# Performance work log

Hardware: AMD Instinct MI355X
Metric: run time of the kernel (lower is better)

Reference implementation:

```python
import jax, jax.numpy as jnp
import numpy as np

B, N, E, H, D, F = 2, 4096, 128, 8, 16, 512
EPS = 1e-6


def _rms_norm(x, w):
    xf = x.astype(jnp.float32)
    n = xf * jax.lax.rsqrt(jnp.mean(xf * xf, axis=-1, keepdims=True) + EPS)
    return n.astype(x.dtype) * w


def setup_inputs() -> dict:
    key = jax.random.key(0)
    ks = jax.random.split(key, 12)
    s = 1.0 / np.sqrt(E)
    sf = 1.0 / np.sqrt(F)
    coords = jax.random.uniform(ks[10], (B, N, 2))
    dis = jnp.sqrt(jnp.sum((coords[:, :, None, :] - coords[:, None, :, :]) ** 2, -1))
    dis = dis * (1.0 - jnp.eye(N))  # zero diagonal
    return {
        "input1": jax.random.normal(ks[0], (B, N, E), jnp.float32),
        "dis_matrix": dis.astype(jnp.float32),
        "Wq": jax.random.uniform(ks[1], (E, E), jnp.float32, -s, s),
        "Wk": jax.random.uniform(ks[2], (E, E), jnp.float32, -s, s),
        "Wv": jax.random.uniform(ks[3], (E, E), jnp.float32, -s, s),
        "alpha": jnp.float32(1.0),
        "ln1_w": jnp.ones((E,), jnp.float32),
        "ln2_w": jnp.ones((E,), jnp.float32),
        "Wcomb": jax.random.uniform(ks[4], (E, E), jnp.float32, -s, s),
        "W1": jax.random.uniform(ks[5], (F, E), jnp.float32, -s, s),
        "b1": jax.random.uniform(ks[6], (F,), jnp.float32, -s, s),
        "W2": jax.random.uniform(ks[7], (E, F), jnp.float32, -sf, sf),
        "b2": jax.random.uniform(ks[8], (E,), jnp.float32, -sf, sf),
    }


def _sparse_attention_afm(x, dis_matrix, Wq, Wk, Wv, alpha):
    # project and split heads: [B,N,E] -> [B,H,N,D]
    def heads(w):
        return (x @ w.T).reshape(B, N, H, D).transpose(0, 2, 1, 3)
    q, k, v = heads(Wq), heads(Wk), heads(Wv)
    log2n = jnp.float32(np.log2(N))
    dis_weight = jnp.exp(-alpha * log2n * dis_matrix)  # [B,N,N] (i,j)
    k_weight = jnp.exp(k)  # [B,H,N,D]
    w1 = jnp.einsum('bij,bhik->bhjk', dis_weight, k_weight * v)
    w2 = jnp.einsum('bij,bhik->bhjk', dis_weight, k_weight)
    out = jax.nn.sigmoid(q) * (w1 / w2)  # [B,H,N,D]
    return out.transpose(0, 2, 1, 3).reshape(B, N, E)


def reference(input1, dis_matrix, Wq, Wk, Wv, alpha, ln1_w, ln2_w, Wcomb, W1, b1, W2, b2):
    h = _rms_norm(input1, ln1_w)
    attn = _sparse_attention_afm(h, dis_matrix, Wq, Wk, Wv, alpha)
    out1 = input1 + attn @ Wcomb.T
    h2 = _rms_norm(out1, ln2_w)
    ffn = jax.nn.relu(h2 @ W1.T + b1) @ W2.T + b2
    return out1 + ffn
```

## Files before the change

### kernel.cpp

```cpp
#include <hip/hip_runtime.h>

#define NTOK 4096
#define BNROWS 8192
#define EDIM 128
#define FDIM 512

typedef __attribute__((ext_vector_type(8))) short bf16x8;
typedef __attribute__((ext_vector_type(4))) float f32x4;

__device__ __forceinline__ ushort f2bf(float x) {
    union { float f; unsigned u; } c; c.f = x;
    unsigned r = c.u + 0x7FFF + ((c.u >> 16) & 1);
    return (ushort)(r >> 16);
}

__global__ void prep_k(const float* __restrict__ Wq, const float* __restrict__ Wk,
                       const float* __restrict__ Wv, const float* __restrict__ Wc,
                       const float* __restrict__ W1, const float* __restrict__ W2,
                       ushort* __restrict__ Wbf,
                       const float* __restrict__ input1, const float* __restrict__ ln1w,
                       ushort* __restrict__ h_bf) {
    const int bx = blockIdx.x, t = threadIdx.x;
    if (bx < 768) {
        int i = bx * 256 + t;
        const float* src; int off;
        if (i < 16384)       { src = Wq; off = i; }
        else if (i < 32768)  { src = Wk; off = i - 16384; }
        else if (i < 49152)  { src = Wv; off = i - 32768; }
        else if (i < 65536)  { src = Wc; off = i - 49152; }
        else if (i < 131072) { src = W1; off = i - 65536; }
        else                 { src = W2; off = i - 131072; }
        Wbf[i] = f2bf(src[off]);
    } else {
        int row  = (bx - 768) * 4 + (t >> 6);
        int lane = t & 63;
        float2 v = ((const float2*)(input1 + (size_t)row * EDIM))[lane];
        float ss = v.x * v.x + v.y * v.y;
#pragma unroll
        for (int off = 32; off > 0; off >>= 1) ss += __shfl_down(ss, off, 64);
        ss = __shfl(ss, 0, 64);
        float r = rsqrtf(ss * (1.0f / 128.0f) + 1e-6f);
        float2 wv = ((const float2*)ln1w)[lane];
        ushort2 o; o.x = f2bf(v.x * r * wv.x); o.y = f2bf(v.y * r * wv.y);
        ((ushort2*)(h_bf + (size_t)row * EDIM))[lane] = o;
    }
}

#define EB_SIGQ  0
#define EB_RELUB 1
#define EB_ACC   2

template<int EPIL>
__device__ __forceinline__ void mgemm_body(
    const ushort* __restrict__ A, int lda,
    const ushort* __restrict__ B, int ldb,
    float* __restrict__ outF, ushort* __restrict__ outB, int Nout, int colbase,
    const float* __restrict__ bias, int M0, int nchunks)
{
    __shared__ ushort As[32 * 136];
    __shared__ ushort Bs[128 * 136];
    const int t = threadIdx.x, lane = t & 63, wv = t >> 6;
    const int m15 = lane & 15, kq = (lane >> 4) * 8;
    const int c0w = wv * 32;
    f32x4 acc[2][2] = {};

    const int ar = t >> 3, as0 = (t & 7) * 2;
    const int br = t >> 1, bs0 = (t & 1) * 8;

    for (int c = 0; c < nchunks; ++c) {
        if (c) __syncthreads();
        int kb = c * 128;
#pragma unroll
        for (int j = 0; j < 2; ++j) {
            int seg = as0 + j;
            *(bf16x8*)&As[ar * 136 + seg * 8] =
                *(const bf16x8*)&A[(size_t)(M0 + ar) * lda + kb + seg * 8];
        }
#pragma unroll
        for (int j = 0; j < 8; ++j) {
            int seg = bs0 + j;
            *(bf16x8*)&Bs[br * 136 + seg * 8] =
                *(const bf16x8*)&B[(size_t)br * ldb + kb + seg * 8];
        }
        __syncthreads();
#pragma unroll
        for (int kc = 0; kc < 4; ++kc) {
            int ko = kc * 32 + kq;
            bf16x8 a0 = *(const bf16x8*)&As[m15 * 136 + ko];
            bf16x8 a1 = *(const bf16x8*)&As[(16 + m15) * 136 + ko];
            bf16x8 b0 = *(const bf16x8*)&Bs[(c0w + m15) * 136 + ko];
            bf16x8 b1 = *(const bf16x8*)&Bs[(c0w + 16 + m15) * 136 + ko];
            acc[0][0] = __builtin_amdgcn_mfma_f32_16x16x32_bf16(a0, b0, acc[0][0], 0, 0, 0);
            acc[0][1] = __builtin_amdgcn_mfma_f32_16x16x32_bf16(a0, b1, acc[0][1], 0, 0, 0);
            acc[1][0] = __builtin_amdgcn_mfma_f32_16x16x32_bf16(a1, b0, acc[1][0], 0, 0, 0);
            acc[1][1] = __builtin_amdgcn_mfma_f32_16x16x32_bf16(a1, b1, acc[1][1], 0, 0, 0);
        }
    }
#pragma unroll
    for (int mi = 0; mi < 2; ++mi)
#pragma unroll
        for (int ni = 0; ni < 2; ++ni)
#pragma unroll
            for (int r = 0; r < 4; ++r) {
                int row = M0 + mi * 16 + (lane >> 4) * 4 + r;
                int lc  = c0w + ni * 16 + m15;
                size_t off = (size_t)row * Nout + colbase + lc;
                float vv = acc[mi][ni][r];
                if (EPIL == EB_SIGQ)  outF[off] = 1.0f / (1.0f + __expf(-vv));
                if (EPIL == EB_RELUB) outB[off] = f2bf(fmaxf(vv + bias[lc], 0.0f));
                if (EPIL == EB_ACC)   outF[off] += vv;
            }
}

__launch_bounds__(256, 3)
__global__ void q_sig_k(const ushort* __restrict__ h, const ushort* __restrict__ Wbf,
                        float* __restrict__ sigq) {
    mgemm_body<EB_SIGQ>(h, 128, Wbf, 128, sigq, nullptr, 128, 0, nullptr,
                        blockIdx.x * 32, 1);
}

__launch_bounds__(256, 3)
__global__ void ffn1_k(const ushort* __restrict__ h2, const ushort* __restrict__ Wbf,
                       const float* __restrict__ b1, ushort* __restrict__ mid) {
    int N0 = blockIdx.y * 128;
    mgemm_body<EB_RELUB>(h2, 128, Wbf + 65536 + N0 * 128, 128, nullptr, mid, 512, N0,
                         b1 + N0, blockIdx.x * 32, 1);
}

__launch_bounds__(256, 3)
__global__ void ffn2_k(const ushort* __restrict__ mid, const ushort* __restrict__ Wbf,
                       float* __restrict__ outp) {
    mgemm_body<EB_ACC>(mid, 512, Wbf + 131072, 512, outp, nullptr, 128, 0, nullptr,
                       blockIdx.x * 32, 4);
}

__launch_bounds__(256, 3)
__global__ void kv_mt_k(const ushort* __restrict__ h, const ushort* __restrict__ Wbf,
                        ushort* __restrict__ Mt) {
    __shared__ ushort As[32 * 136];
    __shared__ ushort Bs[2][64 * 136];
    const int t = threadIdx.x, lane = t & 63, wv = t >> 6;
    const int m15 = lane & 15, quad = lane >> 4, kq = quad * 8;
    const int M0 = blockIdx.x * 32;
    const int e0 = blockIdx.y * 64;

    const int ar = t >> 3, as0 = (t & 7) * 2;
#pragma unroll
    for (int j = 0; j < 2; ++j) {
        int seg = as0 + j;
        *(bf16x8*)&As[ar * 136 + seg * 8] =
            *(const bf16x8*)&h[(size_t)(M0 + ar) * 128 + seg * 8];
    }
    const int bm = t >> 7;
    const int br = (t & 127) >> 1, bs0 = (t & 1) * 8;
    const ushort* W = Wbf + 16384 + bm * 16384;
#pragma unroll
    for (int j = 0; j < 8; ++j) {
        int seg = bs0 + j;
        *(bf16x8*)&Bs[bm][br * 136 + seg * 8] =
            *(const bf16x8*)&W[(size_t)(e0 + br) * 128 + seg * 8];
    }
    __syncthreads();

    f32x4 acck[2] = {}, accv[2] = {};
    const int cw = wv * 16;
#pragma unroll
    for (int kc = 0; kc < 4; ++kc) {
        int ko = kc * 32 + kq;
        bf16x8 a0 = *(const bf16x8*)&As[m15 * 136 + ko];
        bf16x8 a1 = *(const bf16x8*)&As[(16 + m15) * 136 + ko];
        bf16x8 bk = *(const bf16x8*)&Bs[0][(cw + m15) * 136 + ko];
        bf16x8 bv = *(const bf16x8*)&Bs[1][(cw + m15) * 136 + ko];
        acck[0] = __builtin_amdgcn_mfma_f32_16x16x32_bf16(a0, bk, acck[0], 0, 0, 0);
        acck[1] = __builtin_amdgcn_mfma_f32_16x16x32_bf16(a1, bk, acck[1], 0, 0, 0);
        accv[0] = __builtin_amdgcn_mfma_f32_16x16x32_bf16(a0, bv, accv[0], 0, 0, 0);
        accv[1] = __builtin_amdgcn_mfma_f32_16x16x32_bf16(a1, bv, accv[1], 0, 0, 0);
    }
    const int b  = M0 >> 12;
    const int i0 = M0 & (NTOK - 1);
    const int e  = e0 + cw + m15;
    ushort* mt0 = Mt + ((size_t)b * 256 + e) * NTOK;
    ushort* mt1 = Mt + ((size_t)b * 256 + 128 + e) * NTOK;
#pragma unroll
    for (int mi = 0; mi < 2; ++mi) {
        int ib = i0 + mi * 16 + quad * 4;
        ushort4 pv, pk;
        float kw0 = __expf(acck[mi][0]); pv.x = f2bf(kw0 * accv[mi][0]); pk.x = f2bf(kw0);
        float kw1 = __expf(acck[mi][1]); pv.y = f2bf(kw1 * accv[mi][1]); pk.y = f2bf(kw1);
        float kw2 = __expf(acck[mi][2]); pv.z = f2bf(kw2 * accv[mi][2]); pk.z = f2bf(kw2);
        float kw3 = __expf(acck[mi][3]); pv.w = f2bf(kw3 * accv[mi][3]); pk.w = f2bf(kw3);
        *(ushort4*)&mt0[ib] = pv;
        *(ushort4*)&mt1[ib] = pk;
    }
}

__launch_bounds__(256, 2)
__global__ void big_gemm_k(const float* __restrict__ dis, const float* __restrict__ alphap,
                           const ushort* __restrict__ Mt,
                           float* __restrict__ P0, float* __restrict__ P1) {
    __shared__ ushort As[32 * 72];
    __shared__ ushort Bs[256 * 72];
    const int t = threadIdx.x, lane = t & 63, wv = t >> 6;
    const int m15 = lane & 15, quad = lane >> 4, kq = quad * 8;
    const int j0 = blockIdx.x * 32;
    const int b  = blockIdx.y;
    const int s  = blockIdx.z;
    const float coef = -alphap[0] * 12.0f;
    const float* disb = dis + (size_t)b * NTOK * NTOK;
    const ushort* Mtb = Mt + (size_t)b * 256 * NTOK;
    float* outp = ((s == 0) ? P0 : P1) + (size_t)b * NTOK * 256;

    f32x4 acc[2][4] = {};
    const int aj = t >> 3, ak = (t & 7) * 8;
    const int brow = t >> 3, bseg = (t & 7) * 8;
    const int k0 = s * (NTOK / 2);

    float4 fa0, fa1;
    bf16x8 pb[8];
    {
        const float* ap = disb + (size_t)(j0 + aj) * NTOK + k0 + ak;
        fa0 = *(const float4*)ap; fa1 = *(const float4*)(ap + 4);
#pragma unroll
        for (int p = 0; p < 8; ++p)
            pb[p] = *(const bf16x8*)&Mtb[(size_t)(p * 32 + brow) * NTOK + k0 + bseg];
    }

    for (int it = 0; it < 32; ++it) {
        bf16x8 a8;
        a8[0] = (short)f2bf(__expf(coef * fa0.x));
        a8[1] = (short)f2bf(__expf(coef * fa0.y));
        a8[2] = (short)f2bf(__expf(coef * fa0.z));
        a8[3] = (short)f2bf(__expf(coef * fa0.w));
        a8[4] = (short)f2bf(__expf(coef * fa1.x));
        a8[5] = (short)f2bf(__expf(coef * fa1.y));
        a8[6] = (short)f2bf(__expf(coef * fa1.z));
        a8[7] = (short)f2bf(__expf(coef * fa1.w));
        *(bf16x8*)&As[aj * 72 + ak] = a8;
#pragma unroll
        for (int p = 0; p < 8; ++p)
            *(bf16x8*)&Bs[(p * 32 + brow) * 72 + bseg] = pb[p];
        __syncthreads();
        if (it < 31) {
            int kn = k0 + (it + 1) * 64;
            const float* ap = disb + (size_t)(j0 + aj) * NTOK + kn + ak;
            fa0 = *(const float4*)ap; fa1 = *(const float4*)(ap + 4);
#pragma unroll
            for (int p = 0; p < 8; ++p)
                pb[p] = *(const bf16x8*)&Mtb[(size_t)(p * 32 + brow) * NTOK + kn + bseg];
        }
#pragma unroll
        for (int kh = 0; kh < 2; ++kh) {
            int ko = kh * 32 + kq;
            bf16x8 a0 = *(const bf16x8*)&As[m15 * 72 + ko];
            bf16x8 a1 = *(const bf16x8*)&As[(16 + m15) * 72 + ko];
#pragma unroll
            for (int ni = 0; ni < 4; ++ni) {
                bf16x8 bv = *(const bf16x8*)&Bs[(wv * 64 + ni * 16 + m15) * 72 + ko];
                acc[0][ni] = __builtin_amdgcn_mfma_f32_16x16x32_bf16(a0, bv, acc[0][ni], 0, 0, 0);
                acc[1][ni] = __builtin_amdgcn_mfma_f32_16x16x32_bf16(a1, bv, acc[1][ni], 0, 0, 0);
            }
        }
        __syncthreads();
    }
#pragma unroll
    for (int mi = 0; mi < 2; ++mi)
#pragma unroll
        for (int ni = 0; ni < 4; ++ni)
#pragma unroll
            for (int r = 0; r < 4; ++r) {
                int j = j0 + mi * 16 + quad * 4 + r;
                int c = wv * 64 + ni * 16 + m15;
                outp[(size_t)j * 256 + c] = acc[mi][ni][r];
            }
}

__launch_bounds__(256, 2)
__global__ void wcomb_rms2_k(const float* __restrict__ sigq,
                             const float* __restrict__ P0, const float* __restrict__ P1,
                             const ushort* __restrict__ Wbf,
                             const float* __restrict__ input1, const float* __restrict__ b2,
                             const float* __restrict__ ln2w,
                             float* __restrict__ outD, ushort* __restrict__ h2) {
    __shared__ ushort As[32 * 136];
    __shared__ ushort Bs[128 * 136];
    __shared__ float  O[32][132];
    const int t = threadIdx.x, lane = t & 63, wv = t >> 6;
    const int m15 = lane & 15, quad = lane >> 4, kq = quad * 8;
    const int M0 = blockIdx.x * 32;

    {
        const int ar = t >> 3, e0 = (t & 7) * 16;
        const int g = M0 + ar;
        const float4* sg = (const float4*)(sigq + (size_t)g * 128 + e0);
        const float4* p0a = (const float4*)(P0 + (size_t)g * 256 + e0);
        const float4* p1a = (const float4*)(P1 + (size_t)g * 256 + e0);
        const float4* p0b = (const float4*)(P0 + (size_t)g * 256 + 128 + e0);
        const float4* p1b = (const float4*)(P1 + (size_t)g * 256 + 128 + e0);
#pragma unroll
        for (int i = 0; i < 4; ++i) {
            float4 s = sg[i];
            float4 u0 = p0a[i], u1 = p1a[i], d0 = p0b[i], d1 = p1b[i];
            ushort4 a;
            a.x = f2bf(s.x * (u0.x + u1.x) / (d0.x + d1.x));
            a.y = f2bf(s.y * (u0.y + u1.y) / (d0.y + d1.y));
            a.z = f2bf(s.z * (u0.z + u1.z) / (d0.z + d1.z));
            a.w = f2bf(s.w * (u0.w + u1.w) / (d0.w + d1.w));
            *(ushort4*)&As[ar * 136 + e0 + i * 4] = a;
        }
    }
    {
        const int br = t >> 1, bs0 = (t & 1) * 8;
        const ushort* W = Wbf + 49152;
#pragma unroll
        for (int j = 0; j < 8; ++j) {
            int seg = bs0 + j;
            *(bf16x8*)&Bs[br * 136 + seg * 8] =
                *(const bf16x8*)&W[(size_t)br * 128 + seg * 8];
        }
    }
    __syncthreads();

    f32x4 acc[2][2] = {};
    const int c0w = wv * 32;
#pragma unroll
    for (int kc = 0; kc < 4; ++kc) {
        int ko = kc * 32 + kq;
        bf16x8 a0 = *(const bf16x8*)&As[m15 * 136 + ko];
        bf16x8 a1 = *(const bf16x8*)&As[(16 + m15) * 136 + ko];
        bf16x8 b0 = *(const bf16x8*)&Bs[(c0w + m15) * 136 + ko];
        bf16x8 b1 = *(const bf16x8*)&Bs[(c0w + 16 + m15) * 136 + ko];
        acc[0][0] = __builtin_amdgcn_mfma_f32_16x16x32_bf16(a0, b0, acc[0][0], 0, 0, 0);
        acc[0][1] = __builtin_amdgcn_mfma_f32_16x16x32_bf16(a0, b1, acc[0][1], 0, 0, 0);
        acc[1][0] = __builtin_amdgcn_mfma_f32_16x16x32_bf16(a1, b0, acc[1][0], 0, 0, 0);
        acc[1][1] = __builtin_amdgcn_mfma_f32_16x16x32_bf16(a1, b1, acc[1][1], 0, 0, 0);
    }
#pragma unroll
    for (int mi = 0; mi < 2; ++mi)
#pragma unroll
        for (int ni = 0; ni < 2; ++ni)
#pragma unroll
            for (int r = 0; r < 4; ++r) {
                int rl = mi * 16 + quad * 4 + r;
                int col = c0w + ni * 16 + m15;
                size_t off = (size_t)(M0 + rl) * 128 + col;
                float v = acc[mi][ni][r] + input1[off];
                O[rl][col] = v;
                outD[off] = v + b2[col];
            }
    __syncthreads();
    {
        const int row = t >> 3, seg = t & 7;
        float4 x[4];
        float ss = 0.f;
#pragma unroll
        for (int i = 0; i < 4; ++i) {
            x[i] = *(const float4*)&O[row][seg * 16 + i * 4];
            ss += x[i].x * x[i].x + x[i].y * x[i].y + x[i].z * x[i].z + x[i].w * x[i].w;
        }
        ss += __shfl_down(ss, 4, 8);
        ss += __shfl_down(ss, 2, 8);
        ss += __shfl_down(ss, 1, 8);
        ss = __shfl(ss, 0, 8);
        float rr = rsqrtf(ss * (1.0f / 128.0f) + 1e-6f);
        ushort* hp = h2 + (size_t)(M0 + row) * 128 + seg * 16;
#pragma unroll
        for (int i = 0; i < 4; ++i) {
            float4 wv4 = *(const float4*)&ln2w[seg * 16 + i * 4];
            ushort4 o;
            o.x = f2bf(x[i].x * rr * wv4.x);
            o.y = f2bf(x[i].y * rr * wv4.y);
            o.z = f2bf(x[i].z * rr * wv4.z);
            o.w = f2bf(x[i].w * rr * wv4.w);
            *(ushort4*)&hp[i * 4] = o;
        }
    }
}

extern "C" void kernel_launch(void* const* d_in, const int* in_sizes, int n_in,
                              void* d_out, int out_size, void* d_ws, size_t ws_size,
                              hipStream_t stream) {
    const float* input1 = (const float*)d_in[0];
    const float* dis    = (const float*)d_in[1];
    const float* Wq     = (const float*)d_in[2];
    const float* Wk     = (const float*)d_in[3];
    const float* Wv     = (const float*)d_in[4];
    const float* alpha  = (const float*)d_in[5];
    const float* ln1    = (const float*)d_in[6];
    const float* ln2    = (const float*)d_in[7];
    const float* Wcomb  = (const float*)d_in[8];
    const float* W1     = (const float*)d_in[9];
    const float* b1     = (const float*)d_in[10];
    const float* W2     = (const float*)d_in[11];
    const float* b2     = (const float*)d_in[12];
    float* out = (float*)d_out;

    char* w8 = (char*)d_ws;
    ushort* Wbf  = (ushort*)(w8);
    ushort* h_bf = (ushort*)(w8 + (1u << 20));
    float*  sigq = (float*)(w8 + (4u << 20));
    ushort* Mt   = (ushort*)(w8 + (8u << 20));
    float*  P0   = (float*)(w8 + (12u << 20));
    float*  P1   = (float*)(w8 + (20u << 20));
    ushort* h2   = (ushort*)(w8 + (1u << 20));
    ushort* mid  = (ushort*)(w8 + (12u << 20));

    prep_k<<<dim3(2816), 256, 0, stream>>>(Wq, Wk, Wv, Wcomb, W1, W2, Wbf,
                                           input1, ln1, h_bf);
    q_sig_k<<<dim3(256), 256, 0, stream>>>(h_bf, Wbf, sigq);
    kv_mt_k<<<dim3(256, 2), 256, 0, stream>>>(h_bf, Wbf, Mt);
    big_gemm_k<<<dim3(128, 2, 2), 256, 0, stream>>>(dis, alpha, Mt, P0, P1);
    wcomb_rms2_k<<<dim3(256), 256, 0, stream>>>(sigq, P0, P1, Wbf, input1, b2,
                                                ln2, out, h2);
    ffn1_k<<<dim3(256, 4), 256, 0, stream>>>(h2, Wbf, b1, mid);
    ffn2_k<<<dim3(256), 256, 0, stream>>>(mid, Wbf, out);
}
```

Measured before the change: 268.1 us.

## Fuse RMSNorm+QKV projection, fuse FFN, split big GEMM K four ways

Combines the weight conversion, RMSNorm1, Q/K/V projections and sigmoid/exp epilogues into one kernel that converts Wq/Wk/Wv to bf16 on the fly in shared memory. FFN1 and FFN2 are merged into one kernel that keeps the ReLU intermediate in LDS. The distance GEMM splits its reduction into four parts instead of two to double the block count and raise occupancy. The combine kernel now sums four partials. Together this cuts launches and global round trips, at the cost of more partial-sum traffic and redundant per-block weight conversion.

```diff
diff --git a/kernel.cpp b/kernel.cpp
--- a/kernel.cpp
+++ b/kernel.cpp
@@ -14,190 +14,124 @@
     return (ushort)(r >> 16);
 }
 
-__global__ void prep_k(const float* __restrict__ Wq, const float* __restrict__ Wk,
-                       const float* __restrict__ Wv, const float* __restrict__ Wc,
-                       const float* __restrict__ W1, const float* __restrict__ W2,
-                       ushort* __restrict__ Wbf,
-                       const float* __restrict__ input1, const float* __restrict__ ln1w,
-                       ushort* __restrict__ h_bf) {
+__launch_bounds__(256, 1)
+__global__ void qkv_k(const float* __restrict__ input1, const float* __restrict__ ln1w,
+                      const float* __restrict__ Wq, const float* __restrict__ Wk,
+                      const float* __restrict__ Wv, const float* __restrict__ Wc,
+                      const float* __restrict__ W1, const float* __restrict__ W2,
+                      ushort* __restrict__ Wbf, float* __restrict__ sigq,
+                      ushort* __restrict__ Mt) {
     const int bx = blockIdx.x, t = threadIdx.x;
-    if (bx < 768) {
-        int i = bx * 256 + t;
-        const float* src; int off;
-        if (i < 16384)       { src = Wq; off = i; }
-        else if (i < 32768)  { src = Wk; off = i - 16384; }
-        else if (i < 49152)  { src = Wv; off = i - 32768; }
-        else if (i < 65536)  { src = Wc; off = i - 49152; }
-        else if (i < 131072) { src = W1; off = i - 65536; }
-        else                 { src = W2; off = i - 131072; }
-        Wbf[i] = f2bf(src[off]);
-    } else {
-        int row  = (bx - 768) * 4 + (t >> 6);
-        int lane = t & 63;
-        float2 v = ((const float2*)(input1 + (size_t)row * EDIM))[lane];
-        float ss = v.x * v.x + v.y * v.y;
-#pragma unroll
-        for (int off = 32; off > 0; off >>= 1) ss += __shfl_down(ss, off, 64);
-        ss = __shfl(ss, 0, 64);
-        float r = rsqrtf(ss * (1.0f / 128.0f) + 1e-6f);
-        float2 wv = ((const float2*)ln1w)[lane];
-        ushort2 o; o.x = f2bf(v.x * r * wv.x); o.y = f2bf(v.y * r * wv.y);
-        ((ushort2*)(h_bf + (size_t)row * EDIM))[lane] = o;
-    }
-}
-
-#define EB_SIGQ  0
-#define EB_RELUB 1
-#define EB_ACC   2
-
-template<int EPIL>
-__device__ __forceinline__ void mgemm_body(
-    const ushort* __restrict__ A, int lda,
-    const ushort* __restrict__ B, int ldb,
-    float* __restrict__ outF, ushort* __restrict__ outB, int Nout, int colbase,
-    const float* __restrict__ bias, int M0, int nchunks)
-{
+    if (bx >= 256) {
+        int off = (bx - 256) * 1024 + t * 4;
+        const float* src; int o2;
+        if (off < 16384)      { src = Wc; o2 = off; }
+        else if (off < 81920) { src = W1; o2 = off - 16384; }
+        else                  { src = W2; o2 = off - 81920; }
+        float4 f = *(const float4*)(src + o2);
+        ushort4 u; u.x = f2bf(f.x); u.y = f2bf(f.y); u.z = f2bf(f.z); u.w = f2bf(f.w);
+        *(ushort4*)(Wbf + off) = u;
+        return;
+    }
     __shared__ ushort As[32 * 136];
-    __shared__ ushort Bs[128 * 136];
-    const int t = threadIdx.x, lane = t & 63, wv = t >> 6;
-    const int m15 = lane & 15, kq = (lane >> 4) * 8;
+    __shared__ ushort Bs[3][128 * 136];
+    const int lane = t & 63, wv = t >> 6;
+    const int m15 = lane & 15, quad = lane >> 4, kq = quad * 8;
+    const int M0 = bx * 32;
+
+    {
+        const int ar = t >> 3, c0 = (t & 7) * 16;
+        const float* xr = input1 + (size_t)(M0 + ar) * EDIM + c0;
+        float4 x[4];
+        float ss = 0.f;
+#pragma unroll
+        for (int i = 0; i < 4; ++i) {
+            x[i] = ((const float4*)xr)[i];
+            ss += x[i].x * x[i].x + x[i].y * x[i].y + x[i].z * x[i].z + x[i].w * x[i].w;
+        }
+        ss += __shfl_down(ss, 4, 8);
+        ss += __shfl_down(ss, 2, 8);
+        ss += __shfl_down(ss, 1, 8);
+        ss = __shfl(ss, 0, 8);
+        float rr = rsqrtf(ss * (1.0f / 128.0f) + 1e-6f);
+#pragma unroll
+        for (int i = 0; i < 4; ++i) {
+            float4 wv4 = *(const float4*)&ln1w[c0 + i * 4];
+            ushort4 o;
+            o.x = f2bf(x[i].x * rr * wv4.x);
+            o.y = f2bf(x[i].y * rr * wv4.y);
+            o.z = f2bf(x[i].z * rr * wv4.z);
+            o.w = f2bf(x[i].w * rr * wv4.w);
+            *(ushort4*)&As[ar * 136 + c0 + i * 4] = o;
+        }
+    }
+    {
+        const int br = t >> 1, half = (t & 1) * 64;
+        const float* srcs[3] = {Wq, Wk, Wv};
+#pragma unroll
+        for (int m = 0; m < 3; ++m) {
+            const float* wsrc = srcs[m] + (size_t)br * 128 + half;
+#pragma unroll
+            for (int j = 0; j < 8; ++j) {
+                float4 f0 = *(const float4*)(wsrc + j * 8);
+                float4 f1 = *(const float4*)(wsrc + j * 8 + 4);
+                bf16x8 u;
+                u[0] = (short)f2bf(f0.x); u[1] = (short)f2bf(f0.y);
+                u[2] = (short)f2bf(f0.z); u[3] = (short)f2bf(f0.w);
+                u[4] = (short)f2bf(f1.x); u[5] = (short)f2bf(f1.y);
+                u[6] = (short)f2bf(f1.z); u[7] = (short)f2bf(f1.w);
+                *(bf16x8*)&Bs[m][br * 136 + half + j * 8] = u;
+            }
+        }
+    }
+    __syncthreads();
+
+    f32x4 aq[2][2] = {}, ak[2][2] = {}, av[2][2] = {};
     const int c0w = wv * 32;
-    f32x4 acc[2][2] = {};
-
-    const int ar = t >> 3, as0 = (t & 7) * 2;
-    const int br = t >> 1, bs0 = (t & 1) * 8;
-
-    for (int c = 0; c < nchunks; ++c) {
-        if (c) __syncthreads();
-        int kb = c * 128;
-#pragma unroll
-        for (int j = 0; j < 2; ++j) {
-            int seg = as0 + j;
-            *(bf16x8*)&As[ar * 136 + seg * 8] =
-                *(const bf16x8*)&A[(size_t)(M0 + ar) * lda + kb + seg * 8];
-        }
-#pragma unroll
-        for (int j = 0; j < 8; ++j) {
-            int seg = bs0 + j;
-            *(bf16x8*)&Bs[br * 136 + seg * 8] =
-                *(const bf16x8*)&B[(size_t)br * ldb + kb + seg * 8];
-        }
-        __syncthreads();
-#pragma unroll
-        for (int kc = 0; kc < 4; ++kc) {
-            int ko = kc * 32 + kq;
-            bf16x8 a0 = *(const bf16x8*)&As[m15 * 136 + ko];
-            bf16x8 a1 = *(const bf16x8*)&As[(16 + m15) * 136 + ko];
-            bf16x8 b0 = *(const bf16x8*)&Bs[(c0w + m15) * 136 + ko];
-            bf16x8 b1 = *(const bf16x8*)&Bs[(c0w + 16 + m15) * 136 + ko];
-            acc[0][0] = __builtin_amdgcn_mfma_f32_16x16x32_bf16(a0, b0, acc[0][0], 0, 0, 0);
-            acc[0][1] = __builtin_amdgcn_mfma_f32_16x16x32_bf16(a0, b1, acc[0][1], 0, 0, 0);
-            acc[1][0] = __builtin_amdgcn_mfma_f32_16x16x32_bf16(a1, b0, acc[1][0], 0, 0, 0);
-            acc[1][1] = __builtin_amdgcn_mfma_f32_16x16x32_bf16(a1, b1, acc[1][1], 0, 0, 0);
-        }
-    }
-#pragma unroll
-    for (int mi = 0; mi < 2; ++mi)
-#pragma unroll
-        for (int ni = 0; ni < 2; ++ni)
-#pragma unroll
-            for (int r = 0; r < 4; ++r) {
-                int row = M0 + mi * 16 + (lane >> 4) * 4 + r;
-                int lc  = c0w + ni * 16 + m15;
-                size_t off = (size_t)row * Nout + colbase + lc;
-                float vv = acc[mi][ni][r];
-                if (EPIL == EB_SIGQ)  outF[off] = 1.0f / (1.0f + __expf(-vv));
-                if (EPIL == EB_RELUB) outB[off] = f2bf(fmaxf(vv + bias[lc], 0.0f));
-                if (EPIL == EB_ACC)   outF[off] += vv;
-            }
-}
-
-__launch_bounds__(256, 3)
-__global__ void q_sig_k(const ushort* __restrict__ h, const ushort* __restrict__ Wbf,
-                        float* __restrict__ sigq) {
-    mgemm_body<EB_SIGQ>(h, 128, Wbf, 128, sigq, nullptr, 128, 0, nullptr,
-                        blockIdx.x * 32, 1);
-}
-
-__launch_bounds__(256, 3)
-__global__ void ffn1_k(const ushort* __restrict__ h2, const ushort* __restrict__ Wbf,
-                       const float* __restrict__ b1, ushort* __restrict__ mid) {
-    int N0 = blockIdx.y * 128;
-    mgemm_body<EB_RELUB>(h2, 128, Wbf + 65536 + N0 * 128, 128, nullptr, mid, 512, N0,
-                         b1 + N0, blockIdx.x * 32, 1);
-}
-
-__launch_bounds__(256, 3)
-__global__ void ffn2_k(const ushort* __restrict__ mid, const ushort* __restrict__ Wbf,
-                       float* __restrict__ outp) {
-    mgemm_body<EB_ACC>(mid, 512, Wbf + 131072, 512, outp, nullptr, 128, 0, nullptr,
-                       blockIdx.x * 32, 4);
-}
-
-__launch_bounds__(256, 3)
-__global__ void kv_mt_k(const ushort* __restrict__ h, const ushort* __restrict__ Wbf,
-                        ushort* __restrict__ Mt) {
-    __shared__ ushort As[32 * 136];
-    __shared__ ushort Bs[2][64 * 136];
-    const int t = threadIdx.x, lane = t & 63, wv = t >> 6;
-    const int m15 = lane & 15, quad = lane >> 4, kq = quad * 8;
-    const int M0 = blockIdx.x * 32;
-    const int e0 = blockIdx.y * 64;
-
-    const int ar = t >> 3, as0 = (t & 7) * 2;
-#pragma unroll
-    for (int j = 0; j < 2; ++j) {
-        int seg = as0 + j;
-        *(bf16x8*)&As[ar * 136 + seg * 8] =
-            *(const bf16x8*)&h[(size_t)(M0 + ar) * 128 + seg * 8];
-    }
-    const int bm = t >> 7;
-    const int br = (t & 127) >> 1, bs0 = (t & 1) * 8;
-    const ushort* W = Wbf + 16384 + bm * 16384;
-#pragma unroll
-    for (int j = 0; j < 8; ++j) {
-        int seg = bs0 + j;
-        *(bf16x8*)&Bs[bm][br * 136 + seg * 8] =
-            *(const bf16x8*)&W[(size_t)(e0 + br) * 128 + seg * 8];
-    }
-    __syncthreads();
-
-    f32x4 acck[2] = {}, accv[2] = {};
-    const int cw = wv * 16;
 #pragma unroll
     for (int kc = 0; kc < 4; ++kc) {
         int ko = kc * 32 + kq;
         bf16x8 a0 = *(const bf16x8*)&As[m15 * 136 + ko];
         bf16x8 a1 = *(const bf16x8*)&As[(16 + m15) * 136 + ko];
-        bf16x8 bk = *(const bf16x8*)&Bs[0][(cw + m15) * 136 + ko];
-        bf16x8 bv = *(const bf16x8*)&Bs[1][(cw + m15) * 136 + ko];
-        acck[0] = __builtin_amdgcn_mfma_f32_16x16x32_bf16(a0, bk, acck[0], 0, 0, 0);
-        acck[1] = __builtin_amdgcn_mfma_f32_16x16x32_bf16(a1, bk, acck[1], 0, 0, 0);
-        accv[0] = __builtin_amdgcn_mfma_f32_16x16x32_bf16(a0, bv, accv[0], 0, 0, 0);
-        accv[1] = __builtin_amdgcn_mfma_f32_16x16x32_bf16(a1, bv, accv[1], 0, 0, 0);
+#pragma unroll
+        for (int ni = 0; ni < 2; ++ni) {
+            int brow = (c0w + ni * 16 + m15) * 136 + ko;
+            bf16x8 bq = *(const bf16x8*)&Bs[0][brow];
+            bf16x8 bk = *(const bf16x8*)&Bs[1][brow];
+            bf16x8 bv = *(const bf16x8*)&Bs[2][brow];
+            aq[0][ni] = __builtin_amdgcn_mfma_f32_16x16x32_bf16(a0, bq, aq[0][ni], 0, 0, 0);
+            aq[1][ni] = __builtin_amdgcn_mfma_f32_16x16x32_bf16(a1, bq, aq[1][ni], 0, 0, 0);
+            ak[0][ni] = __builtin_amdgcn_mfma_f32_16x16x32_bf16(a0, bk, ak[0][ni], 0, 0, 0);
+            ak[1][ni] = __builtin_amdgcn_mfma_f32_16x16x32_bf16(a1, bk, ak[1][ni], 0, 0, 0);
+            av[0][ni] = __builtin_amdgcn_mfma_f32_16x16x32_bf16(a0, bv, av[0][ni], 0, 0, 0);
+            av[1][ni] = __builtin_amdgcn_mfma_f32_16x16x32_bf16(a1, bv, av[1][ni], 0, 0, 0);
+        }
     }
     const int b  = M0 >> 12;
     const int i0 = M0 & (NTOK - 1);
-    const int e  = e0 + cw + m15;
-    ushort* mt0 = Mt + ((size_t)b * 256 + e) * NTOK;
-    ushort* mt1 = Mt + ((size_t)b * 256 + 128 + e) * NTOK;
-#pragma unroll
-    for (int mi = 0; mi < 2; ++mi) {
-        int ib = i0 + mi * 16 + quad * 4;
-        ushort4 pv, pk;
-        float kw0 = __expf(acck[mi][0]); pv.x = f2bf(kw0 * accv[mi][0]); pk.x = f2bf(kw0);
-        float kw1 = __expf(acck[mi][1]); pv.y = f2bf(kw1 * accv[mi][1]); pk.y = f2bf(kw1);
-        float kw2 = __expf(acck[mi][2]); pv.z = f2bf(kw2 * accv[mi][2]); pk.z = f2bf(kw2);
-        float kw3 = __expf(acck[mi][3]); pv.w = f2bf(kw3 * accv[mi][3]); pk.w = f2bf(kw3);
-        *(ushort4*)&mt0[ib] = pv;
-        *(ushort4*)&mt1[ib] = pk;
-    }
-}
-
-__launch_bounds__(256, 2)
+#pragma unroll
+    for (int mi = 0; mi < 2; ++mi)
+#pragma unroll
+        for (int ni = 0; ni < 2; ++ni) {
+            int e  = c0w + ni * 16 + m15;
+            int ib = i0 + mi * 16 + quad * 4;
+#pragma unroll
+            for (int r = 0; r < 4; ++r)
+                sigq[(size_t)(M0 + mi * 16 + quad * 4 + r) * EDIM + e] =
+                    1.0f / (1.0f + __expf(-aq[mi][ni][r]));
+            ushort4 pv, pk;
+            float k0 = __expf(ak[mi][ni][0]); pv.x = f2bf(k0 * av[mi][ni][0]); pk.x = f2bf(k0);
+            float k1 = __expf(ak[mi][ni][1]); pv.y = f2bf(k1 * av[mi][ni][1]); pk.y = f2bf(k1);
+            float k2 = __expf(ak[mi][ni][2]); pv.z = f2bf(k2 * av[mi][ni][2]); pk.z = f2bf(k2);
+            float k3 = __expf(ak[mi][ni][3]); pv.w = f2bf(k3 * av[mi][ni][3]); pk.w = f2bf(k3);
+            *(ushort4*)&Mt[((size_t)b * 256 + e) * NTOK + ib]       = pv;
+            *(ushort4*)&Mt[((size_t)b * 256 + 128 + e) * NTOK + ib] = pk;
+        }
+}
+
+__launch_bounds__(256, 3)
 __global__ void big_gemm_k(const float* __restrict__ dis, const float* __restrict__ alphap,
-                           const ushort* __restrict__ Mt,
-                           float* __restrict__ P0, float* __restrict__ P1) {
+                           const ushort* __restrict__ Mt, float* __restrict__ P) {
     __shared__ ushort As[32 * 72];
     __shared__ ushort Bs[256 * 72];
     const int t = threadIdx.x, lane = t & 63, wv = t >> 6;
@@ -208,12 +142,13 @@
     const float coef = -alphap[0] * 12.0f;
     const float* disb = dis + (size_t)b * NTOK * NTOK;
     const ushort* Mtb = Mt + (size_t)b * 256 * NTOK;
-    float* outp = ((s == 0) ? P0 : P1) + (size_t)b * NTOK * 256;
+    float* outp = P + ((size_t)(s * 2 + b) * NTOK + j0) * 256;
 
     f32x4 acc[2][4] = {};
     const int aj = t >> 3, ak = (t & 7) * 8;
     const int brow = t >> 3, bseg = (t & 7) * 8;
-    const int k0 = s * (NTOK / 2);
+    const int k0 = s * (NTOK / 4);
+    const int nIter = (NTOK / 4) / 64;
 
     float4 fa0, fa1;
     bf16x8 pb[8];
@@ -225,7 +160,7 @@
             pb[p] = *(const bf16x8*)&Mtb[(size_t)(p * 32 + brow) * NTOK + k0 + bseg];
     }
 
-    for (int it = 0; it < 32; ++it) {
+    for (int it = 0; it < nIter; ++it) {
         bf16x8 a8;
         a8[0] = (short)f2bf(__expf(coef * fa0.x));
         a8[1] = (short)f2bf(__expf(coef * fa0.y));
@@ -240,7 +175,7 @@
         for (int p = 0; p < 8; ++p)
             *(bf16x8*)&Bs[(p * 32 + brow) * 72 + bseg] = pb[p];
         __syncthreads();
-        if (it < 31) {
+        if (it < nIter - 1) {
             int kn = k0 + (it + 1) * 64;
             const float* ap = disb + (size_t)(j0 + aj) * NTOK + kn + ak;
             fa0 = *(const float4*)ap; fa1 = *(const float4*)(ap + 4);
@@ -268,15 +203,14 @@
         for (int ni = 0; ni < 4; ++ni)
 #pragma unroll
             for (int r = 0; r < 4; ++r) {
-                int j = j0 + mi * 16 + quad * 4 + r;
+                int j = mi * 16 + quad * 4 + r;
                 int c = wv * 64 + ni * 16 + m15;
                 outp[(size_t)j * 256 + c] = acc[mi][ni][r];
             }
 }
 
 __launch_bounds__(256, 2)
-__global__ void wcomb_rms2_k(const float* __restrict__ sigq,
-                             const float* __restrict__ P0, const float* __restrict__ P1,
+__global__ void wcomb_rms2_k(const float* __restrict__ sigq, const float* __restrict__ P,
                              const ushort* __restrict__ Wbf,
                              const float* __restrict__ input1, const float* __restrict__ b2,
                              const float* __restrict__ ln2w,
@@ -291,32 +225,37 @@
     {
         const int ar = t >> 3, e0 = (t & 7) * 16;
         const int g = M0 + ar;
-        const float4* sg = (const float4*)(sigq + (size_t)g * 128 + e0);
-        const float4* p0a = (const float4*)(P0 + (size_t)g * 256 + e0);
-        const float4* p1a = (const float4*)(P1 + (size_t)g * 256 + e0);
-        const float4* p0b = (const float4*)(P0 + (size_t)g * 256 + 128 + e0);
-        const float4* p1b = (const float4*)(P1 + (size_t)g * 256 + 128 + e0);
+        const int b = g >> 12, j = g & (NTOK - 1);
+        const float* sg = sigq + (size_t)g * 128 + e0;
+        const float* Pg0 = P + ((size_t)(0 + b) * NTOK + j) * 256 + e0;
+        const float* Pg1 = P + ((size_t)(2 + b) * NTOK + j) * 256 + e0;
+        const float* Pg2 = P + ((size_t)(4 + b) * NTOK + j) * 256 + e0;
+        const float* Pg3 = P + ((size_t)(6 + b) * NTOK + j) * 256 + e0;
 #pragma unroll
         for (int i = 0; i < 4; ++i) {
-            float4 s = sg[i];
-            float4 u0 = p0a[i], u1 = p1a[i], d0 = p0b[i], d1 = p1b[i];
+            float4 s = *(const float4*)(sg + i * 4);
+            float4 n0 = *(const float4*)(Pg0 + i * 4);
+            float4 n1 = *(const float4*)(Pg1 + i * 4);
+            float4 n2 = *(const float4*)(Pg2 + i * 4);
+            float4 n3 = *(const float4*)(Pg3 + i * 4);
+            float4 d0 = *(const float4*)(Pg0 + 128 + i * 4);
+            float4 d1 = *(const float4*)(Pg1 + 128 + i * 4);
+            float4 d2 = *(const float4*)(Pg2 + 128 + i * 4);
+            float4 d3 = *(const float4*)(Pg3 + 128 + i * 4);
             ushort4 a;
-            a.x = f2bf(s.x * (u0.x + u1.x) / (d0.x + d1.x));
-            a.y = f2bf(s.y * (u0.y + u1.y) / (d0.y + d1.y));
-            a.z = f2bf(s.z * (u0.z + u1.z) / (d0.z + d1.z));
-            a.w = f2bf(s.w * (u0.w + u1.w) / (d0.w + d1.w));
+            a.x = f2bf(s.x * (n0.x + n1.x + n2.x + n3.x) / (d0.x + d1.x + d2.x + d3.x));
+            a.y = f2bf(s.y * (n0.y + n1.y + n2.y + n3.y) / (d0.y + d1.y + d2.y + d3.y));
+            a.z = f2bf(s.z * (n0.z + n1.z + n2.z + n3.z) / (d0.z + d1.z + d2.z + d3.z));
+            a.w = f2bf(s.w * (n0.w + n1.w + n2.w + n3.w) / (d0.w + d1.w + d2.w + d3.w));
             *(ushort4*)&As[ar * 136 + e0 + i * 4] = a;
         }
     }
     {
-        const int br = t >> 1, bs0 = (t & 1) * 8;
-        const ushort* W = Wbf + 49152;
-#pragma unroll
-        for (int j = 0; j < 8; ++j) {
-            int seg = bs0 + j;
-            *(bf16x8*)&Bs[br * 136 + seg * 8] =
-                *(const bf16x8*)&W[(size_t)br * 128 + seg * 8];
-        }
+        const int br = t >> 1, half = (t & 1) * 64;
+#pragma unroll
+        for (int j = 0; j < 8; ++j)
+            *(bf16x8*)&Bs[br * 136 + half + j * 8] =
+                *(const bf16x8*)&Wbf[(size_t)br * 128 + half + j * 8];
     }
     __syncthreads();
 
@@ -374,6 +313,92 @@
             *(ushort4*)&hp[i * 4] = o;
         }
     }
+}
+
+__launch_bounds__(256, 2)
+__global__ void ffn_k(const ushort* __restrict__ h2, const ushort* __restrict__ Wbf,
+                      const float* __restrict__ b1, float* __restrict__ out) {
+    __shared__ ushort As[32 * 136];
+    __shared__ ushort Am[32 * 520];
+    __shared__ ushort Bs[128 * 136];
+    const int t = threadIdx.x, lane = t & 63, wv = t >> 6;
+    const int m15 = lane & 15, quad = lane >> 4, kq = quad * 8;
+    const int M0 = blockIdx.x * 32;
+    const int c0w = wv * 32;
+    const int br = t >> 1, half = (t & 1) * 64;
+    const ushort* W1bf = Wbf + 16384;
+    const ushort* W2bf = Wbf + 81920;
+
+    {
+        const int ar = t >> 3, a0 = (t & 7) * 16;
+        *(bf16x8*)&As[ar * 136 + a0]     = *(const bf16x8*)&h2[(size_t)(M0 + ar) * 128 + a0];
+        *(bf16x8*)&As[ar * 136 + a0 + 8] = *(const bf16x8*)&h2[(size_t)(M0 + ar) * 128 + a0 + 8];
+    }
+    for (int fc = 0; fc < 4; ++fc) {
+        __syncthreads();
+#pragma unroll
+        for (int j = 0; j < 8; ++j)
+            *(bf16x8*)&Bs[br * 136 + half + j * 8] =
+                *(const bf16x8*)&W1bf[(size_t)(fc * 128 + br) * 128 + half + j * 8];
+        __syncthreads();
+        f32x4 acc[2][2] = {};
+#pragma unroll
+        for (int kc = 0; kc < 4; ++kc) {
+            int ko = kc * 32 + kq;
+            bf16x8 a0 = *(const bf16x8*)&As[m15 * 136 + ko];
+            bf16x8 a1 = *(const bf16x8*)&As[(16 + m15) * 136 + ko];
+            bf16x8 b0 = *(const bf16x8*)&Bs[(c0w + m15) * 136 + ko];
+            bf16x8 b1v = *(const bf16x8*)&Bs[(c0w + 16 + m15) * 136 + ko];
+            acc[0][0] = __builtin_amdgcn_mfma_f32_16x16x32_bf16(a0, b0, acc[0][0], 0, 0, 0);
+            acc[0][1] = __builtin_amdgcn_mfma_f32_16x16x32_bf16(a0, b1v, acc[0][1], 0, 0, 0);
+            acc[1][0] = __builtin_amdgcn_mfma_f32_16x16x32_bf16(a1, b0, acc[1][0], 0, 0, 0);
+            acc[1][1] = __builtin_amdgcn_mfma_f32_16x16x32_bf16(a1, b1v, acc[1][1], 0, 0, 0);
+        }
+#pragma unroll
+        for (int mi = 0; mi < 2; ++mi)
+#pragma unroll
+            for (int ni = 0; ni < 2; ++ni)
+#pragma unroll
+                for (int r = 0; r < 4; ++r) {
+                    int row = mi * 16 + quad * 4 + r;
+                    int col = c0w + ni * 16 + m15;
+                    Am[row * 520 + fc * 128 + col] =
+                        f2bf(fmaxf(acc[mi][ni][r] + b1[fc * 128 + col], 0.0f));
+                }
+    }
+    f32x4 acc2[2][2] = {};
+    for (int kc = 0; kc < 4; ++kc) {
+        __syncthreads();
+#pragma unroll
+        for (int j = 0; j < 8; ++j)
+            *(bf16x8*)&Bs[br * 136 + half + j * 8] =
+                *(const bf16x8*)&W2bf[(size_t)br * 512 + kc * 128 + half + j * 8];
+        __syncthreads();
+#pragma unroll
+        for (int kk = 0; kk < 4; ++kk) {
+            int koA = kc * 128 + kk * 32 + kq;
+            int koB = kk * 32 + kq;
+            bf16x8 a0 = *(const bf16x8*)&Am[m15 * 520 + koA];
+            bf16x8 a1 = *(const bf16x8*)&Am[(16 + m15) * 520 + koA];
+            bf16x8 b0 = *(const bf16x8*)&Bs[(c0w + m15) * 136 + koB];
+            bf16x8 b1v = *(const bf16x8*)&Bs[(c0w + 16 + m15) * 136 + koB];
+            acc2[0][0] = __builtin_amdgcn_mfma_f32_16x16x32_bf16(a0, b0, acc2[0][0], 0, 0, 0);
+            acc2[0][1] = __builtin_amdgcn_mfma_f32_16x16x32_bf16(a0, b1v, acc2[0][1], 0, 0, 0);
+            acc2[1][0] = __builtin_amdgcn_mfma_f32_16x16x32_bf16(a1, b0, acc2[1][0], 0, 0, 0);
+            acc2[1][1] = __builtin_amdgcn_mfma_f32_16x16x32_bf16(a1, b1v, acc2[1][1], 0, 0, 0);
+        }
+    }
+#pragma unroll
+    for (int mi = 0; mi < 2; ++mi)
+#pragma unroll
+        for (int ni = 0; ni < 2; ++ni)
+#pragma unroll
+            for (int r = 0; r < 4; ++r) {
+                int row = M0 + mi * 16 + quad * 4 + r;
+                int col = c0w + ni * 16 + m15;
+                size_t off = (size_t)row * 128 + col;
+                out[off] += acc2[mi][ni][r];
+            }
 }
 
 extern "C" void kernel_launch(void* const* d_in, const int* in_sizes, int n_in,
@@ -396,21 +421,14 @@
 
     char* w8 = (char*)d_ws;
     ushort* Wbf  = (ushort*)(w8);
-    ushort* h_bf = (ushort*)(w8 + (1u << 20));
     float*  sigq = (float*)(w8 + (4u << 20));
     ushort* Mt   = (ushort*)(w8 + (8u << 20));
-    float*  P0   = (float*)(w8 + (12u << 20));
-    float*  P1   = (float*)(w8 + (20u << 20));
-    ushort* h2   = (ushort*)(w8 + (1u << 20));
-    ushort* mid  = (ushort*)(w8 + (12u << 20));
-
-    prep_k<<<dim3(2816), 256, 0, stream>>>(Wq, Wk, Wv, Wcomb, W1, W2, Wbf,
-                                           input1, ln1, h_bf);
-    q_sig_k<<<dim3(256), 256, 0, stream>>>(h_bf, Wbf, sigq);
-    kv_mt_k<<<dim3(256, 2), 256, 0, stream>>>(h_bf, Wbf, Mt);
-    big_gemm_k<<<dim3(128, 2, 2), 256, 0, stream>>>(dis, alpha, Mt, P0, P1);
-    wcomb_rms2_k<<<dim3(256), 256, 0, stream>>>(sigq, P0, P1, Wbf, input1, b2,
-                                                ln2, out, h2);
-    ffn1_k<<<dim3(256, 4), 256, 0, stream>>>(h2, Wbf, b1, mid);
-    ffn2_k<<<dim3(256), 256, 0, stream>>>(mid, Wbf, out);
-}
+    ushort* h2   = (ushort*)(w8 + (12u << 20));
+    float*  P    = (float*)(w8 + (16u << 20));
+
+    qkv_k<<<dim3(400), 256, 0, stream>>>(input1, ln1, Wq, Wk, Wv, Wcomb, W1, W2,
+                                         Wbf, sigq, Mt);
+    big_gemm_k<<<dim3(128, 2, 4), 256, 0, stream>>>(dis, alpha, Mt, P);
+    wcomb_rms2_k<<<dim3(256), 256, 0, stream>>>(sigq, P, Wbf, input1, b2, ln2, out, h2);
+    ffn_k<<<dim3(256), 256, 0, stream>>>(h2, Wbf, b1, out);
+}
```

Result: slower. 280.0 us (+4.4%).
